# Optimization experiments

Measured on AMD Instinct MI355X. Metric: run time of the kernel, lower is better.

Reference implementation:

```python
import jax, jax.numpy as jnp
import numpy as np

BS, NQ, L = 64, 900, 1024
LANG_DIM, HID = 768, 256
N_EXP, TOP_K = 8, 2
MOE_W = 0.5
LOG_SCALE0 = 0.0
PRIOR_PROB = 0.01
BIAS0 = -np.log((1.0 - PRIOR_PROB) / PRIOR_PROB)  # -log((1-p)/p)


def setup_inputs() -> dict:
    key = jax.random.key(0)
    ks = jax.random.split(key, 8)
    s_in = 1.0 / np.sqrt(LANG_DIM)
    return {
        "x": jax.random.normal(ks[0], (BS, NQ, HID), jnp.float32),
        "embedding": jax.random.normal(ks[1], (BS, L, LANG_DIM), jnp.float32),
        "proj_w": jax.random.uniform(ks[2], (LANG_DIM, HID), jnp.float32, -s_in, s_in),
        "proj_b": jnp.zeros((HID,), jnp.float32),
        "gate_w": jax.random.uniform(ks[3], (LANG_DIM, N_EXP), jnp.float32, -s_in, s_in),
        "gate_b": jnp.zeros((N_EXP,), jnp.float32),
        "expert_w": jax.random.uniform(ks[4], (N_EXP, LANG_DIM, HID), jnp.float32, -s_in, s_in),
        "expert_b": jnp.zeros((N_EXP, HID), jnp.float32),
        "bias_lang": jnp.zeros((LANG_DIM,), jnp.float32),
        "bias0": jnp.array([BIAS0], jnp.float32),
        "log_scale": jnp.array([LOG_SCALE0], jnp.float32),
    }


def _moe(emb, gate_w, gate_b, expert_w, expert_b):
    # emb: (bs, L, lang_dim)
    gate_logits = emb @ gate_w + gate_b              # (bs, L, E)
    gate_weights = jax.nn.softmax(gate_logits, axis=-1)
    topv, topi = jax.lax.top_k(gate_weights, TOP_K)  # (bs, L, k)
    # dense combine weights: scatter top-k probs back to (bs, L, E)
    combine = jnp.sum(jax.nn.one_hot(topi, N_EXP, dtype=emb.dtype) * topv[..., None], axis=-2)
    out = jnp.zeros(emb.shape[:-1] + (HID,), emb.dtype)
    for e in range(N_EXP):  # small fixed expert count; dense per-expert GEMM
        out = out + combine[..., e:e + 1] * (emb @ expert_w[e] + expert_b[e])
    return out


def reference(x, embedding, proj_w, proj_b, gate_w, gate_b,
              expert_w, expert_b, bias_lang, bias0, log_scale):
    emb = embedding / jnp.linalg.norm(embedding, axis=-1, keepdims=True)
    tokens = emb @ proj_w + proj_b                        # (bs, L, HID)
    moe_out = _moe(emb, gate_w, gate_b, expert_w, expert_b)
    tokens = (1.0 - MOE_W) * tokens + MOE_W * moe_out
    token_bias = emb @ bias_lang + bias0[0]               # (bs, L)
    logit = jnp.einsum('bqh,blh->bql', x, tokens) / jnp.exp(log_scale[0])
    logit = logit + token_bias[:, None, :]
    logit = jnp.clip(logit, -50000.0, 50000.0)
    return logit
```

## Files before the change

kernel.cpp:

```cpp
#include <hip/hip_runtime.h>
#include <hip/hip_bf16.h>


typedef __attribute__((ext_vector_type(8))) short bf16x8;
typedef __attribute__((ext_vector_type(4))) float f32x4;

#define NROW 65536
#define CAP  65536
#define CSTRIDE 16
#define SWZ(r) ((((r) & 3) ^ (((r) >> 2) & 3)))

__device__ __forceinline__ unsigned short f2bf(float f) {
    unsigned u = __builtin_bit_cast(unsigned, f);
    u += 0x7fffu + ((u >> 16) & 1u);
    return (unsigned short)(u >> 16);
}
__device__ __forceinline__ float bf2f(unsigned short h) {
    unsigned u = ((unsigned)h) << 16;
    return __builtin_bit_cast(float, u);
}
__device__ __forceinline__ void gload16(const void* g, void* l) {
    __builtin_amdgcn_global_load_lds(
        (const __attribute__((address_space(1))) void*)g,
        (__attribute__((address_space(3))) void*)l, 16, 0, 0);
}
__device__ __forceinline__ unsigned cvt_pk_bf16(float a, float b) {
    unsigned r;
    asm("v_cvt_pk_bf16_f32 %0, %1, %2" : "=v"(r) : "v"(a), "v"(b));
    return r;
}

__global__ __launch_bounds__(256) void kx_cast(
    const float* __restrict__ x, unsigned short* __restrict__ x_bf)
{
    int i = blockIdx.x * 256 + threadIdx.x;
    float4 v = ((const float4*)x)[i];
    unsigned long long o = (unsigned long long)cvt_pk_bf16(v.x, v.y) |
                           ((unsigned long long)cvt_pk_bf16(v.z, v.w) << 32);
    __builtin_nontemporal_store(o, (unsigned long long*)x_bf + i);
}

__global__ __launch_bounds__(256) void k0_wT(
    const float* __restrict__ proj_w, const float* __restrict__ expert_w,
    unsigned short* __restrict__ wcatT)
{
    int j = blockIdx.z;
    int d0 = blockIdx.x * 64, h0 = blockIdx.y * 64;
    const float* W = (j < 8) ? expert_w + (size_t)j * 768 * 256 : proj_w;
    __shared__ unsigned short s[64][65];
    int t = threadIdx.x;
    #pragma unroll
    for (int i = 0; i < 16; i++) {
        int d = i * 4 + (t >> 6), h = t & 63;
        s[d][h] = f2bf(W[(size_t)(d0 + d) * 256 + h0 + h]);
    }
    __syncthreads();
    #pragma unroll
    for (int i = 0; i < 16; i++) {
        int h = i * 4 + (t >> 6), d = t & 63;
        wcatT[(size_t)(j * 256 + h0 + h) * 768 + d0 + d] = s[d][h];
    }
}

__global__ __launch_bounds__(256) void kz_misc(
    const float* __restrict__ proj_b, const float* __restrict__ expert_b,
    float* __restrict__ bcat, unsigned* __restrict__ cnt)
{
    int i = blockIdx.x * 256 + threadIdx.x;
    if (i < 2304) {
        int jj = i >> 8, h = i & 255;
        bcat[i] = (jj < 8) ? expert_b[jj * 256 + h] : proj_b[h];
    }
    if (i < 8 * CSTRIDE) cnt[i] = 0;
}

__global__ __launch_bounds__(256, 4) void k1_fused(
    const float* __restrict__ emb_in, const float* __restrict__ gate_w,
    const float* __restrict__ gate_b, const float* __restrict__ bias_lang,
    const float* __restrict__ bias0, unsigned short* __restrict__ emb_bf,
    unsigned* __restrict__ top2, float2* __restrict__ c2,
    float* __restrict__ tbias)
{
    __shared__ float gwT[9 * 768];
    for (int i = threadIdx.x; i < 768 * 8; i += 256) {
        int d = i >> 3, e = i & 7;
        gwT[e * 768 + d] = gate_w[i];
    }
    for (int i = threadIdx.x; i < 768; i += 256)
        gwT[8 * 768 + i] = bias_lang[i];
    __syncthreads();

    int w = threadIdx.x >> 6, lane = threadIdx.x & 63;
    #pragma unroll 1
    for (int it = 0; it < 8; ++it) {
        int r = blockIdx.x * 32 + w * 8 + it;
        const float4* rv = (const float4*)(emb_in + (size_t)r * 768);
        float4 v0 = rv[lane], v1 = rv[lane + 64], v2 = rv[lane + 128];
        float ss = v0.x*v0.x + v0.y*v0.y + v0.z*v0.z + v0.w*v0.w
                 + v1.x*v1.x + v1.y*v1.y + v1.z*v1.z + v1.w*v1.w
                 + v2.x*v2.x + v2.y*v2.y + v2.z*v2.z + v2.w*v2.w;
        #pragma unroll
        for (int m = 1; m < 64; m <<= 1) ss += __shfl_xor(ss, m, 64);
        float rn = rsqrtf(ss);

        unsigned long long q0 = (unsigned long long)cvt_pk_bf16(v0.x*rn, v0.y*rn) |
                                ((unsigned long long)cvt_pk_bf16(v0.z*rn, v0.w*rn) << 32);
        unsigned long long q1 = (unsigned long long)cvt_pk_bf16(v1.x*rn, v1.y*rn) |
                                ((unsigned long long)cvt_pk_bf16(v1.z*rn, v1.w*rn) << 32);
        unsigned long long q2 = (unsigned long long)cvt_pk_bf16(v2.x*rn, v2.y*rn) |
                                ((unsigned long long)cvt_pk_bf16(v2.z*rn, v2.w*rn) << 32);
        unsigned long long* ob = (unsigned long long*)(emb_bf + (size_t)r * 768);
        __builtin_nontemporal_store(q0, ob + lane);
        __builtin_nontemporal_store(q1, ob + lane + 64);
        __builtin_nontemporal_store(q2, ob + lane + 128);

        float acc[9];
        #pragma unroll
        for (int i = 0; i < 9; i++) acc[i] = 0.f;
        const float4 vv[3] = { v0, v1, v2 };
        #pragma unroll
        for (int k = 0; k < 3; k++) {
            float4 v = vv[k];
            #pragma unroll
            for (int e = 0; e < 9; e++) {
                float4 g = *(const float4*)&gwT[e * 768 + k * 256 + lane * 4];
                acc[e] += v.x*g.x + v.y*g.y + v.z*g.z + v.w*g.w;
            }
        }
        #pragma unroll
        for (int m = 1; m < 64; m <<= 1) {
            #pragma unroll
            for (int i = 0; i < 9; i++) acc[i] += __shfl_xor(acc[i], m, 64);
        }
        if (lane == 0) {
            float g[8];
            #pragma unroll
            for (int e = 0; e < 8; e++) g[e] = acc[e] * rn + gate_b[e];
            float mx = g[0];
            #pragma unroll
            for (int e = 1; e < 8; e++) mx = fmaxf(mx, g[e]);
            float p[8], s = 0.f;
            #pragma unroll
            for (int e = 0; e < 8; e++) { p[e] = __expf(g[e] - mx); s += p[e]; }
            float inv = 0.5f / s;
            int i1 = 0;
            #pragma unroll
            for (int e = 1; e < 8; e++) if (g[e] > g[i1]) i1 = e;
            int i2 = (i1 == 0) ? 1 : 0;
            #pragma unroll
            for (int e = 0; e < 8; e++) if (e != i1 && g[e] > g[i2]) i2 = e;
            top2[r] = (unsigned)i1 | ((unsigned)i2 << 8);
            c2[r]   = make_float2(p[i1] * inv, p[i2] * inv);
            tbias[r] = acc[8] * rn + bias0[0];
        }
    }
}

__global__ __launch_bounds__(256) void kb_bucket(
    const unsigned* __restrict__ top2, const float2* __restrict__ c2,
    unsigned* __restrict__ cnt, unsigned* __restrict__ bidx,
    float* __restrict__ bscale)
{
    __shared__ unsigned lcnt[8];
    __shared__ unsigned gbase[8];
    int tid = threadIdx.x, lane = tid & 63;
    if (tid < 8) lcnt[tid] = 0;
    __syncthreads();
    int r = blockIdx.x * 256 + tid;
    unsigned t = top2[r];
    float2 c = c2[r];
    int ii[2] = { (int)(t & 255), (int)((t >> 8) & 255) };
    float cc[2] = { c.x, c.y };
    unsigned lpos[2];
    #pragma unroll
    for (int slot = 0; slot < 2; slot++) {
        int myE = ii[slot];
        #pragma unroll 1
        for (int e = 0; e < 8; e++) {
            unsigned long long mask = __ballot(myE == e);
            if (myE == e) {
                int leader = __ffsll((unsigned long long)mask) - 1;
                unsigned base = 0;
                if (lane == leader)
                    base = atomicAdd(&lcnt[e], (unsigned)__popcll(mask));
                base = __shfl(base, leader, 64);
                lpos[slot] = base + (unsigned)__popcll(mask & ((1ull << lane) - 1ull));
            }
        }
    }
    __syncthreads();
    if (tid < 8) gbase[tid] = atomicAdd(&cnt[tid * CSTRIDE], lcnt[tid]);
    __syncthreads();
    #pragma unroll
    for (int slot = 0; slot < 2; slot++) {
        int e = ii[slot];
        unsigned p = gbase[e] + lpos[slot];
        bidx[(size_t)e * CAP + p]   = (unsigned)r | ((unsigned)slot << 16);
        bscale[(size_t)e * CAP + p] = cc[slot];
    }
}

__global__ __launch_bounds__(512, 2) void k2_expert(
    const unsigned short* __restrict__ emb_bf, const unsigned short* __restrict__ wcatT,
    const float* __restrict__ bcat, const unsigned* __restrict__ cnt,
    const unsigned* __restrict__ bidx, const float* __restrict__ bscale,
    unsigned short* __restrict__ partial)
{
    int e = blockIdx.y;
    int tile = blockIdx.x;
    int cnt_e = (int)cnt[e * CSTRIDE];
    if (tile * 128 >= cnt_e) return;
    int tid = threadIdx.x, lane = tid & 63, w = tid >> 6;
    int wm = w >> 2, wn = w & 3;
    __shared__ __align__(16) unsigned short As[2][128 * 32];
    __shared__ __align__(16) unsigned short Bs[2][256 * 32];
    __shared__ unsigned sRow[128];
    __shared__ float sScale[128];
    if (tid < 128) {
        int gi = tile * 128 + tid;
        unsigned rs; float sc;
        if (gi < cnt_e) { rs = bidx[(size_t)e * CAP + gi];
                          sc = bscale[(size_t)e * CAP + gi]; }
        else            { rs = 0; sc = 0.f; }
        sRow[tid] = rs; sScale[tid] = sc;
    }
    __syncthreads();
    int r16 = lane & 15, r4 = lane >> 4;
    int srowA = tid >> 2, ssegA = (tid & 3) ^ SWZ(srowA);
    const unsigned short* aSrc =
        emb_bf + (size_t)(sRow[srowA] & 0xFFFFu) * 768 + ssegA * 8;
    const unsigned short* bBase = wcatT + (size_t)e * 256 * 768;

    auto stageA = [&](int kt, int buf) {
        gload16(aSrc + kt * 32, &As[buf][w * 512]);
    };
    auto stageB = [&](int kt, int buf) {
        #pragma unroll
        for (int i = 0; i < 2; i++) {
            int u = i * 512 + tid;
            int brow = u >> 2, seg = (u & 3) ^ SWZ(brow);
            gload16(&bBase[(size_t)brow * 768 + kt * 32 + seg * 8],
                    &Bs[buf][i * 4096 + w * 512]);
        }
    };

    f32x4 acc[4][4];
    #pragma unroll
    for (int mi = 0; mi < 4; mi++)
        #pragma unroll
        for (int ni = 0; ni < 4; ni++) acc[mi][ni] = f32x4{0.f, 0.f, 0.f, 0.f};

    stageA(0, 0); stageB(0, 0);
    __syncthreads();
    int buf = 0;
    #pragma unroll 1
    for (int kt = 0; kt < 24; ++kt) {
        if (kt < 23) { stageA(kt + 1, buf ^ 1); stageB(kt + 1, buf ^ 1); }
        bf16x8 a[4], b[4];
        #pragma unroll
        for (int mi = 0; mi < 4; mi++) {
            int arow = wm * 64 + mi * 16 + r16;
            a[mi] = *(const bf16x8*)&As[buf][arow * 32 + (r4 ^ SWZ(arow)) * 8];
        }
        #pragma unroll
        for (int ni = 0; ni < 4; ni++) {
            int brow = wn * 64 + ni * 16 + r16;
            b[ni] = *(const bf16x8*)&Bs[buf][brow * 32 + (r4 ^ SWZ(brow)) * 8];
        }
        #pragma unroll
        for (int mi = 0; mi < 4; mi++)
            #pragma unroll
            for (int ni = 0; ni < 4; ni++)
                acc[mi][ni] = __builtin_amdgcn_mfma_f32_16x16x32_bf16(
                    a[mi], b[ni], acc[mi][ni], 0, 0, 0);
        __syncthreads();
        buf ^= 1;
    }

    float bj[4];
    #pragma unroll
    for (int ni = 0; ni < 4; ni++) bj[ni] = bcat[e * 256 + wn * 64 + ni * 16 + r16];
    #pragma unroll
    for (int mi = 0; mi < 4; mi++) {
        #pragma unroll
        for (int e4 = 0; e4 < 4; e4++) {
            int rl = wm * 64 + mi * 16 + r4 * 4 + e4;
            if (tile * 128 + rl < cnt_e) {
                unsigned rs = sRow[rl];
                float sc = sScale[rl];
                unsigned rowg = rs & 0xFFFFu, slot = rs >> 16;
                #pragma unroll
                for (int ni = 0; ni < 4; ni++) {
                    int col = wn * 64 + ni * 16 + r16;
                    __builtin_nontemporal_store(
                        f2bf(sc * (acc[mi][ni][e4] + bj[ni])),
                        &partial[((size_t)slot * NROW + rowg) * 256 + col]);
                }
            }
        }
    }
}

__global__ __launch_bounds__(512, 2) void k2_proj(
    const unsigned short* __restrict__ emb_bf, const unsigned short* __restrict__ wcatT,
    const float* __restrict__ bcat, const unsigned short* __restrict__ partial,
    unsigned short* __restrict__ tokens)
{
    int tile = blockIdx.x;
    int tid = threadIdx.x, lane = tid & 63, w = tid >> 6;
    int wm = w >> 2, wn = w & 3;
    int rowBase = tile * 128;
    __shared__ __align__(16) unsigned short As[2][128 * 32];
    __shared__ __align__(16) unsigned short Bs[2][256 * 32];
    int r16 = lane & 15, r4 = lane >> 4;
    int srowA = tid >> 2, ssegA = (tid & 3) ^ SWZ(srowA);
    const unsigned short* aSrc =
        emb_bf + (size_t)(rowBase + srowA) * 768 + ssegA * 8;
    const unsigned short* bBase = wcatT + (size_t)8 * 256 * 768;

    auto stageA = [&](int kt, int buf) {
        gload16(aSrc + kt * 32, &As[buf][w * 512]);
    };
    auto stageB = [&](int kt, int buf) {
        #pragma unroll
        for (int i = 0; i < 2; i++) {
            int u = i * 512 + tid;
            int brow = u >> 2, seg = (u & 3) ^ SWZ(brow);
            gload16(&bBase[(size_t)brow * 768 + kt * 32 + seg * 8],
                    &Bs[buf][i * 4096 + w * 512]);
        }
    };

    f32x4 acc[4][4];
    #pragma unroll
    for (int mi = 0; mi < 4; mi++)
        #pragma unroll
        for (int ni = 0; ni < 4; ni++) acc[mi][ni] = f32x4{0.f, 0.f, 0.f, 0.f};

    stageA(0, 0); stageB(0, 0);
    __syncthreads();
    int buf = 0;
    #pragma unroll 1
    for (int kt = 0; kt < 24; ++kt) {
        if (kt < 23) { stageA(kt + 1, buf ^ 1); stageB(kt + 1, buf ^ 1); }
        bf16x8 a[4], b[4];
        #pragma unroll
        for (int mi = 0; mi < 4; mi++) {
            int arow = wm * 64 + mi * 16 + r16;
            a[mi] = *(const bf16x8*)&As[buf][arow * 32 + (r4 ^ SWZ(arow)) * 8];
        }
        #pragma unroll
        for (int ni = 0; ni < 4; ni++) {
            int brow = wn * 64 + ni * 16 + r16;
            b[ni] = *(const bf16x8*)&Bs[buf][brow * 32 + (r4 ^ SWZ(brow)) * 8];
        }
        #pragma unroll
        for (int mi = 0; mi < 4; mi++)
            #pragma unroll
            for (int ni = 0; ni < 4; ni++)
                acc[mi][ni] = __builtin_amdgcn_mfma_f32_16x16x32_bf16(
                    a[mi], b[ni], acc[mi][ni], 0, 0, 0);
        __syncthreads();
        buf ^= 1;
    }

    const size_t S = (size_t)NROW * 256;
    float bj[4];
    #pragma unroll
    for (int ni = 0; ni < 4; ni++) bj[ni] = bcat[8 * 256 + wn * 64 + ni * 16 + r16];
    #pragma unroll
    for (int mi = 0; mi < 4; mi++) {
        #pragma unroll
        for (int e4 = 0; e4 < 4; e4++) {
            int rl = wm * 64 + mi * 16 + r4 * 4 + e4;
            size_t rowg = rowBase + rl;
            #pragma unroll
            for (int ni = 0; ni < 4; ni++) {
                int col = wn * 64 + ni * 16 + r16;
                float p0 = bf2f(partial[rowg * 256 + col]);
                float p1 = bf2f(partial[S + rowg * 256 + col]);
                float v = 0.5f * (acc[mi][ni][e4] + bj[ni]) + p0 + p1;
                __builtin_nontemporal_store(f2bf(v), &tokens[rowg * 256 + col]);
            }
        }
    }
}

__global__ __launch_bounds__(256, 4) void k3_logit(
    const unsigned short* __restrict__ x_bf, const unsigned short* __restrict__ tokens,
    const float* __restrict__ tbias, const float* __restrict__ log_scale,
    float* __restrict__ out)
{
    int tid = threadIdx.x, lane = tid & 63, w = tid >> 6;
    int wm = w >> 1, wn = w & 1;
    int tn = blockIdx.x, tm = blockIdx.y, b = blockIdx.z;
    __shared__ __align__(16) unsigned short As[2][128 * 32];
    __shared__ __align__(16) unsigned short Bs[2][128 * 32];
    const unsigned short* A = x_bf + (size_t)b * 900 * 256;
    const unsigned short* B = tokens + (size_t)b * 1024 * 256;
    f32x4 acc[4][4];
    #pragma unroll
    for (int mi = 0; mi < 4; mi++)
        #pragma unroll
        for (int ni = 0; ni < 4; ni++) acc[mi][ni] = f32x4{0.f, 0.f, 0.f, 0.f};
    int r16 = lane & 15, r4 = lane >> 4;

    auto stage = [&](int kt, int buf) {
        #pragma unroll
        for (int i = 0; i < 2; i++) {
            int u = i * 256 + tid;
            int row = u >> 2, seg = (u & 3) ^ SWZ(row);
            int ar = tm * 128 + row;
            if (ar > 899) ar = 899;
            gload16(&A[(size_t)ar * 256 + kt * 32 + seg * 8],
                    &As[buf][i * 2048 + w * 512]);
            int nr = tn * 128 + row;
            gload16(&B[(size_t)nr * 256 + kt * 32 + seg * 8],
                    &Bs[buf][i * 2048 + w * 512]);
        }
    };

    stage(0, 0);
    __syncthreads();
    int buf = 0;
    #pragma unroll 1
    for (int kt = 0; kt < 8; ++kt) {
        if (kt < 7) stage(kt + 1, buf ^ 1);
        bf16x8 a[4], bb[4];
        #pragma unroll
        for (int mi = 0; mi < 4; mi++) {
            int row = wm * 64 + mi * 16 + r16;
            a[mi] = *(const bf16x8*)&As[buf][row * 32 + (r4 ^ SWZ(row)) * 8];
        }
        #pragma unroll
        for (int ni = 0; ni < 4; ni++) {
            int row = wn * 64 + ni * 16 + r16;
            bb[ni] = *(const bf16x8*)&Bs[buf][row * 32 + (r4 ^ SWZ(row)) * 8];
        }
        #pragma unroll
        for (int mi = 0; mi < 4; mi++)
            #pragma unroll
            for (int ni = 0; ni < 4; ni++)
                acc[mi][ni] = __builtin_amdgcn_mfma_f32_16x16x32_bf16(
                    a[mi], bb[ni], acc[mi][ni], 0, 0, 0);
        __syncthreads();
        buf ^= 1;
    }
    float inv = __expf(-log_scale[0]);
    #pragma unroll
    for (int ni = 0; ni < 4; ni++) {
        int l = tn * 128 + wn * 64 + ni * 16 + r16;
        float tbv = tbias[b * 1024 + l];
        #pragma unroll
        for (int mi = 0; mi < 4; mi++) {
            #pragma unroll
            for (int e = 0; e < 4; e++) {
                int q = tm * 128 + wm * 64 + mi * 16 + r4 * 4 + e;
                if (q < 900) {
                    float vv = acc[mi][ni][e] * inv + tbv;
                    vv = fminf(fmaxf(vv, -50000.f), 50000.f);
                    __builtin_nontemporal_store(
                        vv, &out[((size_t)b * 900 + q) * 1024 + l]);
                }
            }
        }
    }
}

extern "C" void kernel_launch(void* const* d_in, const int* in_sizes, int n_in,
                              void* d_out, int out_size, void* d_ws, size_t ws_size,
                              hipStream_t stream)
{
    const float* x         = (const float*)d_in[0];
    const float* embedding = (const float*)d_in[1];
    const float* proj_w    = (const float*)d_in[2];
    const float* proj_b    = (const float*)d_in[3];
    const float* gate_w    = (const float*)d_in[4];
    const float* gate_b    = (const float*)d_in[5];
    const float* expert_w  = (const float*)d_in[6];
    const float* expert_b  = (const float*)d_in[7];
    const float* bias_lang = (const float*)d_in[8];
    const float* bias0     = (const float*)d_in[9];
    const float* log_scale = (const float*)d_in[10];
    float* out = (float*)d_out;

    size_t off = 0;
    char* base = (char*)d_ws;
    auto alloc = [&](size_t bytes) -> void* {
        void* p = base + off;
        off += (bytes + 255) & ~(size_t)255;
        return p;
    };
    unsigned short* emb_bf  = (unsigned short*)alloc((size_t)NROW * 768 * 2);
    unsigned short* x_bf    = (unsigned short*)alloc((size_t)14745600 * 2);
    unsigned short* wcatT   = (unsigned short*)alloc((size_t)2304 * 768 * 2);
    float* bcat             = (float*)alloc(2304 * 4);
    float* tbias            = (float*)alloc((size_t)NROW * 4);
    unsigned short* tokens  = (unsigned short*)alloc((size_t)NROW * 256 * 2);
    unsigned* cnt           = (unsigned*)alloc(8 * CSTRIDE * 4);
    unsigned* top2          = (unsigned*)alloc((size_t)NROW * 4);
    float2* c2              = (float2*)alloc((size_t)NROW * 8);
    unsigned* bidx          = (unsigned*)alloc((size_t)8 * CAP * 4);
    float* bscale           = (float*)alloc((size_t)8 * CAP * 4);
    unsigned short* partial = (unsigned short*)alloc((size_t)2 * NROW * 256 * 2);

    kx_cast<<<14400, 256, 0, stream>>>(x, x_bf);
    dim3 gt(12, 4, 9);
    k0_wT<<<gt, 256, 0, stream>>>(proj_w, expert_w, wcatT);
    kz_misc<<<9, 256, 0, stream>>>(proj_b, expert_b, bcat, cnt);
    k1_fused<<<2048, 256, 0, stream>>>(embedding, gate_w, gate_b, bias_lang, bias0,
                                       emb_bf, top2, c2, tbias);
    kb_bucket<<<NROW / 256, 256, 0, stream>>>(top2, c2, cnt, bidx, bscale);
    dim3 g2(512, 8);
    k2_expert<<<g2, 512, 0, stream>>>(emb_bf, wcatT, bcat, cnt, bidx, bscale, partial);
    k2_proj<<<512, 512, 0, stream>>>(emb_bf, wcatT, bcat, partial, tokens);
    dim3 g3(8, 8, 64);
    k3_logit<<<g3, 256, 0, stream>>>(x_bf, tokens, tbias, log_scale, out);
}
```

Measured before the change: 393.8 us.

## Enlarge GEMM block tiles to 256 rows in expert, proj and logit kernels

Doubles the M tile of the expert and projection GEMMs from 128 to 256 rows. Each warp now holds 8x4 accumulators, and A fragments are loaded inside the mi loop. The logit kernel moves from 128x128 tiles with 256 threads to 256x256 tiles with 512 threads. The aim is to raise operand reuse per LDS load and cut global traffic per output. The cost is higher register and LDS use, fewer blocks (hurting occupancy and tail balance on sparse expert buckets), and more wasted work on the padded 900-row edge of the logit GEMM.

```diff
diff --git a/kernel.cpp b/kernel.cpp
--- a/kernel.cpp
+++ b/kernel.cpp
@@ -209,15 +209,18 @@
     int e = blockIdx.y;
     int tile = blockIdx.x;
     int cnt_e = (int)cnt[e * CSTRIDE];
-    if (tile * 128 >= cnt_e) return;
+    if (tile * 256 >= cnt_e) return;
     int tid = threadIdx.x, lane = tid & 63, w = tid >> 6;
     int wm = w >> 2, wn = w & 3;
-    __shared__ __align__(16) unsigned short As[2][128 * 32];
+    __shared__ __align__(16) unsigned short As[2][256 * 32];
     __shared__ __align__(16) unsigned short Bs[2][256 * 32];
-    __shared__ unsigned sRow[128];
-    __shared__ float sScale[128];
-    if (tid < 128) {
-        int gi = tile * 128 + tid;
+    __shared__ unsigned sRow[256];
+    __shared__ float sScale[256];
+    #pragma unroll
+    for (int i = 0; i < 1; i++) {
+    }
+    if (tid < 256) {
+        int gi = tile * 256 + tid;
         unsigned rs; float sc;
         if (gi < cnt_e) { rs = bidx[(size_t)e * CAP + gi];
                           sc = bscale[(size_t)e * CAP + gi]; }
@@ -226,13 +229,17 @@
     }
     __syncthreads();
     int r16 = lane & 15, r4 = lane >> 4;
-    int srowA = tid >> 2, ssegA = (tid & 3) ^ SWZ(srowA);
-    const unsigned short* aSrc =
-        emb_bf + (size_t)(sRow[srowA] & 0xFFFFu) * 768 + ssegA * 8;
+    int row0 = tid >> 2, row1 = 128 + (tid >> 2);
+    int seg0 = (tid & 3) ^ SWZ(row0), seg1 = (tid & 3) ^ SWZ(row1);
+    const unsigned short* aSrc0 =
+        emb_bf + (size_t)(sRow[row0] & 0xFFFFu) * 768 + seg0 * 8;
+    const unsigned short* aSrc1 =
+        emb_bf + (size_t)(sRow[row1] & 0xFFFFu) * 768 + seg1 * 8;
     const unsigned short* bBase = wcatT + (size_t)e * 256 * 768;
 
     auto stageA = [&](int kt, int buf) {
-        gload16(aSrc + kt * 32, &As[buf][w * 512]);
+        gload16(aSrc0 + kt * 32, &As[buf][w * 512]);
+        gload16(aSrc1 + kt * 32, &As[buf][4096 + w * 512]);
     };
     auto stageB = [&](int kt, int buf) {
         #pragma unroll
@@ -244,9 +251,9 @@
         }
     };
 
-    f32x4 acc[4][4];
-    #pragma unroll
-    for (int mi = 0; mi < 4; mi++)
+    f32x4 acc[8][4];
+    #pragma unroll
+    for (int mi = 0; mi < 8; mi++)
         #pragma unroll
         for (int ni = 0; ni < 4; ni++) acc[mi][ni] = f32x4{0.f, 0.f, 0.f, 0.f};
 
@@ -256,23 +263,21 @@
     #pragma unroll 1
     for (int kt = 0; kt < 24; ++kt) {
         if (kt < 23) { stageA(kt + 1, buf ^ 1); stageB(kt + 1, buf ^ 1); }
-        bf16x8 a[4], b[4];
-        #pragma unroll
-        for (int mi = 0; mi < 4; mi++) {
-            int arow = wm * 64 + mi * 16 + r16;
-            a[mi] = *(const bf16x8*)&As[buf][arow * 32 + (r4 ^ SWZ(arow)) * 8];
-        }
+        bf16x8 b[4];
         #pragma unroll
         for (int ni = 0; ni < 4; ni++) {
             int brow = wn * 64 + ni * 16 + r16;
             b[ni] = *(const bf16x8*)&Bs[buf][brow * 32 + (r4 ^ SWZ(brow)) * 8];
         }
         #pragma unroll
-        for (int mi = 0; mi < 4; mi++)
+        for (int mi = 0; mi < 8; mi++) {
+            int arow = wm * 128 + mi * 16 + r16;
+            bf16x8 a = *(const bf16x8*)&As[buf][arow * 32 + (r4 ^ SWZ(arow)) * 8];
             #pragma unroll
             for (int ni = 0; ni < 4; ni++)
                 acc[mi][ni] = __builtin_amdgcn_mfma_f32_16x16x32_bf16(
-                    a[mi], b[ni], acc[mi][ni], 0, 0, 0);
+                    a, b[ni], acc[mi][ni], 0, 0, 0);
+        }
         __syncthreads();
         buf ^= 1;
     }
@@ -281,11 +286,11 @@
     #pragma unroll
     for (int ni = 0; ni < 4; ni++) bj[ni] = bcat[e * 256 + wn * 64 + ni * 16 + r16];
     #pragma unroll
-    for (int mi = 0; mi < 4; mi++) {
+    for (int mi = 0; mi < 8; mi++) {
         #pragma unroll
         for (int e4 = 0; e4 < 4; e4++) {
-            int rl = wm * 64 + mi * 16 + r4 * 4 + e4;
-            if (tile * 128 + rl < cnt_e) {
+            int rl = wm * 128 + mi * 16 + r4 * 4 + e4;
+            if (tile * 256 + rl < cnt_e) {
                 unsigned rs = sRow[rl];
                 float sc = sScale[rl];
                 unsigned rowg = rs & 0xFFFFu, slot = rs >> 16;
@@ -309,17 +314,21 @@
     int tile = blockIdx.x;
     int tid = threadIdx.x, lane = tid & 63, w = tid >> 6;
     int wm = w >> 2, wn = w & 3;
-    int rowBase = tile * 128;
-    __shared__ __align__(16) unsigned short As[2][128 * 32];
+    int rowBase = tile * 256;
+    __shared__ __align__(16) unsigned short As[2][256 * 32];
     __shared__ __align__(16) unsigned short Bs[2][256 * 32];
     int r16 = lane & 15, r4 = lane >> 4;
-    int srowA = tid >> 2, ssegA = (tid & 3) ^ SWZ(srowA);
-    const unsigned short* aSrc =
-        emb_bf + (size_t)(rowBase + srowA) * 768 + ssegA * 8;
+    int row0 = tid >> 2, row1 = 128 + (tid >> 2);
+    int seg0 = (tid & 3) ^ SWZ(row0), seg1 = (tid & 3) ^ SWZ(row1);
+    const unsigned short* aSrc0 =
+        emb_bf + (size_t)(rowBase + row0) * 768 + seg0 * 8;
+    const unsigned short* aSrc1 =
+        emb_bf + (size_t)(rowBase + row1) * 768 + seg1 * 8;
     const unsigned short* bBase = wcatT + (size_t)8 * 256 * 768;
 
     auto stageA = [&](int kt, int buf) {
-        gload16(aSrc + kt * 32, &As[buf][w * 512]);
+        gload16(aSrc0 + kt * 32, &As[buf][w * 512]);
+        gload16(aSrc1 + kt * 32, &As[buf][4096 + w * 512]);
     };
     auto stageB = [&](int kt, int buf) {
         #pragma unroll
@@ -331,9 +340,9 @@
         }
     };
 
-    f32x4 acc[4][4];
-    #pragma unroll
-    for (int mi = 0; mi < 4; mi++)
+    f32x4 acc[8][4];
+    #pragma unroll
+    for (int mi = 0; mi < 8; mi++)
         #pragma unroll
         for (int ni = 0; ni < 4; ni++) acc[mi][ni] = f32x4{0.f, 0.f, 0.f, 0.f};
 
@@ -343,23 +352,21 @@
     #pragma unroll 1
     for (int kt = 0; kt < 24; ++kt) {
         if (kt < 23) { stageA(kt + 1, buf ^ 1); stageB(kt + 1, buf ^ 1); }
-        bf16x8 a[4], b[4];
-        #pragma unroll
-        for (int mi = 0; mi < 4; mi++) {
-            int arow = wm * 64 + mi * 16 + r16;
-            a[mi] = *(const bf16x8*)&As[buf][arow * 32 + (r4 ^ SWZ(arow)) * 8];
-        }
+        bf16x8 b[4];
         #pragma unroll
         for (int ni = 0; ni < 4; ni++) {
             int brow = wn * 64 + ni * 16 + r16;
             b[ni] = *(const bf16x8*)&Bs[buf][brow * 32 + (r4 ^ SWZ(brow)) * 8];
         }
         #pragma unroll
-        for (int mi = 0; mi < 4; mi++)
+        for (int mi = 0; mi < 8; mi++) {
+            int arow = wm * 128 + mi * 16 + r16;
+            bf16x8 a = *(const bf16x8*)&As[buf][arow * 32 + (r4 ^ SWZ(arow)) * 8];
             #pragma unroll
             for (int ni = 0; ni < 4; ni++)
                 acc[mi][ni] = __builtin_amdgcn_mfma_f32_16x16x32_bf16(
-                    a[mi], b[ni], acc[mi][ni], 0, 0, 0);
+                    a, b[ni], acc[mi][ni], 0, 0, 0);
+        }
         __syncthreads();
         buf ^= 1;
     }
@@ -369,10 +376,10 @@
     #pragma unroll
     for (int ni = 0; ni < 4; ni++) bj[ni] = bcat[8 * 256 + wn * 64 + ni * 16 + r16];
     #pragma unroll
-    for (int mi = 0; mi < 4; mi++) {
+    for (int mi = 0; mi < 8; mi++) {
         #pragma unroll
         for (int e4 = 0; e4 < 4; e4++) {
-            int rl = wm * 64 + mi * 16 + r4 * 4 + e4;
+            int rl = wm * 128 + mi * 16 + r4 * 4 + e4;
             size_t rowg = rowBase + rl;
             #pragma unroll
             for (int ni = 0; ni < 4; ni++) {
@@ -386,21 +393,21 @@
     }
 }
 
-__global__ __launch_bounds__(256, 4) void k3_logit(
+__global__ __launch_bounds__(512, 2) void k3_logit(
     const unsigned short* __restrict__ x_bf, const unsigned short* __restrict__ tokens,
     const float* __restrict__ tbias, const float* __restrict__ log_scale,
     float* __restrict__ out)
 {
     int tid = threadIdx.x, lane = tid & 63, w = tid >> 6;
-    int wm = w >> 1, wn = w & 1;
+    int wm = w >> 2, wn = w & 3;
     int tn = blockIdx.x, tm = blockIdx.y, b = blockIdx.z;
-    __shared__ __align__(16) unsigned short As[2][128 * 32];
-    __shared__ __align__(16) unsigned short Bs[2][128 * 32];
+    __shared__ __align__(16) unsigned short As[2][256 * 32];
+    __shared__ __align__(16) unsigned short Bs[2][256 * 32];
     const unsigned short* A = x_bf + (size_t)b * 900 * 256;
     const unsigned short* B = tokens + (size_t)b * 1024 * 256;
-    f32x4 acc[4][4];
-    #pragma unroll
-    for (int mi = 0; mi < 4; mi++)
+    f32x4 acc[8][4];
+    #pragma unroll
+    for (int mi = 0; mi < 8; mi++)
         #pragma unroll
         for (int ni = 0; ni < 4; ni++) acc[mi][ni] = f32x4{0.f, 0.f, 0.f, 0.f};
     int r16 = lane & 15, r4 = lane >> 4;
@@ -408,15 +415,15 @@
     auto stage = [&](int kt, int buf) {
         #pragma unroll
         for (int i = 0; i < 2; i++) {
-            int u = i * 256 + tid;
+            int u = i * 512 + tid;
             int row = u >> 2, seg = (u & 3) ^ SWZ(row);
-            int ar = tm * 128 + row;
+            int ar = tm * 256 + row;
             if (ar > 899) ar = 899;
             gload16(&A[(size_t)ar * 256 + kt * 32 + seg * 8],
-                    &As[buf][i * 2048 + w * 512]);
-            int nr = tn * 128 + row;
+                    &As[buf][i * 4096 + w * 512]);
+            int nr = tn * 256 + row;
             gload16(&B[(size_t)nr * 256 + kt * 32 + seg * 8],
-                    &Bs[buf][i * 2048 + w * 512]);
+                    &Bs[buf][i * 4096 + w * 512]);
         }
     };
 
@@ -426,36 +433,34 @@
     #pragma unroll 1
     for (int kt = 0; kt < 8; ++kt) {
         if (kt < 7) stage(kt + 1, buf ^ 1);
-        bf16x8 a[4], bb[4];
-        #pragma unroll
-        for (int mi = 0; mi < 4; mi++) {
-            int row = wm * 64 + mi * 16 + r16;
-            a[mi] = *(const bf16x8*)&As[buf][row * 32 + (r4 ^ SWZ(row)) * 8];
-        }
+        bf16x8 bb[4];
         #pragma unroll
         for (int ni = 0; ni < 4; ni++) {
             int row = wn * 64 + ni * 16 + r16;
             bb[ni] = *(const bf16x8*)&Bs[buf][row * 32 + (r4 ^ SWZ(row)) * 8];
         }
         #pragma unroll
-        for (int mi = 0; mi < 4; mi++)
+        for (int mi = 0; mi < 8; mi++) {
+            int row = wm * 128 + mi * 16 + r16;
+            bf16x8 a = *(const bf16x8*)&As[buf][row * 32 + (r4 ^ SWZ(row)) * 8];
             #pragma unroll
             for (int ni = 0; ni < 4; ni++)
                 acc[mi][ni] = __builtin_amdgcn_mfma_f32_16x16x32_bf16(
-                    a[mi], bb[ni], acc[mi][ni], 0, 0, 0);
+                    a, bb[ni], acc[mi][ni], 0, 0, 0);
+        }
         __syncthreads();
         buf ^= 1;
     }
     float inv = __expf(-log_scale[0]);
     #pragma unroll
     for (int ni = 0; ni < 4; ni++) {
-        int l = tn * 128 + wn * 64 + ni * 16 + r16;
+        int l = tn * 256 + wn * 64 + ni * 16 + r16;
         float tbv = tbias[b * 1024 + l];
         #pragma unroll
-        for (int mi = 0; mi < 4; mi++) {
+        for (int mi = 0; mi < 8; mi++) {
             #pragma unroll
             for (int e = 0; e < 4; e++) {
-                int q = tm * 128 + wm * 64 + mi * 16 + r4 * 4 + e;
+                int q = tm * 256 + wm * 128 + mi * 16 + r4 * 4 + e;
                 if (q < 900) {
                     float vv = acc[mi][ni][e] * inv + tbv;
                     vv = fminf(fmaxf(vv, -50000.f), 50000.f);
@@ -511,9 +516,9 @@
     k1_fused<<<2048, 256, 0, stream>>>(embedding, gate_w, gate_b, bias_lang, bias0,
                                        emb_bf, top2, c2, tbias);
     kb_bucket<<<NROW / 256, 256, 0, stream>>>(top2, c2, cnt, bidx, bscale);
-    dim3 g2(512, 8);
+    dim3 g2(256, 8);
     k2_expert<<<g2, 512, 0, stream>>>(emb_bf, wcatT, bcat, cnt, bidx, bscale, partial);
-    k2_proj<<<512, 512, 0, stream>>>(emb_bf, wcatT, bcat, partial, tokens);
-    dim3 g3(8, 8, 64);
-    k3_logit<<<g3, 256, 0, stream>>>(x_bf, tokens, tbias, log_scale, out);
-}
+    k2_proj<<<256, 512, 0, stream>>>(emb_bf, wcatT, bcat, partial, tokens);
+    dim3 g3(4, 4, 64);
+    k3_logit<<<g3, 512, 0, stream>>>(x_bf, tokens, tbias, log_scale, out);
+}
```

Result: slower. 412.2 us (+4.7%).

## Restructure logit GEMM to keep A fragments in registers and stream B directly

Applied to the files above, without the earlier changes.

Rewrites k3_logit so each block handles 64 query rows and all 1024 tokens. Each wave keeps the full K=256 A fragments in registers and streams token rows straight from global memory in 32-column chunks, with no LDS staging and no block syncs. This removes the LDS round-trip and barrier overhead and reads x only once per query tile. In exchange it adds register pressure, lowering occupancy to 2 blocks per SIMD, and B loads become uncoalesced global reads that depend on cache.

```diff
diff --git a/kernel.cpp b/kernel.cpp
--- a/kernel.cpp
+++ b/kernel.cpp
@@ -386,81 +386,67 @@
     }
 }
 
-__global__ __launch_bounds__(256, 4) void k3_logit(
+__global__ __launch_bounds__(256, 2) void k3_logit(
     const unsigned short* __restrict__ x_bf, const unsigned short* __restrict__ tokens,
     const float* __restrict__ tbias, const float* __restrict__ log_scale,
     float* __restrict__ out)
 {
-    int tid = threadIdx.x, lane = tid & 63, w = tid >> 6;
-    int wm = w >> 1, wn = w & 1;
-    int tn = blockIdx.x, tm = blockIdx.y, b = blockIdx.z;
-    __shared__ __align__(16) unsigned short As[2][128 * 32];
-    __shared__ __align__(16) unsigned short Bs[2][128 * 32];
+    int lane = threadIdx.x & 63, w = threadIdx.x >> 6;
+    int tm = blockIdx.x, b = blockIdx.y;
+    int r16 = lane & 15, r4 = lane >> 4;
+    int qBase = tm * 64;
     const unsigned short* A = x_bf + (size_t)b * 900 * 256;
-    const unsigned short* B = tokens + (size_t)b * 1024 * 256;
-    f32x4 acc[4][4];
-    #pragma unroll
-    for (int mi = 0; mi < 4; mi++)
-        #pragma unroll
-        for (int ni = 0; ni < 4; ni++) acc[mi][ni] = f32x4{0.f, 0.f, 0.f, 0.f};
-    int r16 = lane & 15, r4 = lane >> 4;
-
-    auto stage = [&](int kt, int buf) {
-        #pragma unroll
-        for (int i = 0; i < 2; i++) {
-            int u = i * 256 + tid;
-            int row = u >> 2, seg = (u & 3) ^ SWZ(row);
-            int ar = tm * 128 + row;
-            if (ar > 899) ar = 899;
-            gload16(&A[(size_t)ar * 256 + kt * 32 + seg * 8],
-                    &As[buf][i * 2048 + w * 512]);
-            int nr = tn * 128 + row;
-            gload16(&B[(size_t)nr * 256 + kt * 32 + seg * 8],
-                    &Bs[buf][i * 2048 + w * 512]);
-        }
-    };
-
-    stage(0, 0);
-    __syncthreads();
-    int buf = 0;
+    const unsigned short* B = tokens + ((size_t)b * 1024 + (size_t)w * 256) * 256;
+
+    bf16x8 af[4][8];
+    #pragma unroll
+    for (int mi = 0; mi < 4; mi++) {
+        int q = qBase + mi * 16 + r16;
+        if (q > 899) q = 899;
+        const unsigned short* ap = A + (size_t)q * 256 + r4 * 8;
+        #pragma unroll
+        for (int kt = 0; kt < 8; kt++)
+            af[mi][kt] = *(const bf16x8*)(ap + kt * 32);
+    }
+    float inv = __expf(-log_scale[0]);
+
     #pragma unroll 1
-    for (int kt = 0; kt < 8; ++kt) {
-        if (kt < 7) stage(kt + 1, buf ^ 1);
-        bf16x8 a[4], bb[4];
-        #pragma unroll
-        for (int mi = 0; mi < 4; mi++) {
-            int row = wm * 64 + mi * 16 + r16;
-            a[mi] = *(const bf16x8*)&As[buf][row * 32 + (r4 ^ SWZ(row)) * 8];
-        }
-        #pragma unroll
-        for (int ni = 0; ni < 4; ni++) {
-            int row = wn * 64 + ni * 16 + r16;
-            bb[ni] = *(const bf16x8*)&Bs[buf][row * 32 + (r4 ^ SWZ(row)) * 8];
-        }
+    for (int c = 0; c < 8; c++) {
+        f32x4 acc[4][2];
         #pragma unroll
         for (int mi = 0; mi < 4; mi++)
             #pragma unroll
-            for (int ni = 0; ni < 4; ni++)
-                acc[mi][ni] = __builtin_amdgcn_mfma_f32_16x16x32_bf16(
-                    a[mi], bb[ni], acc[mi][ni], 0, 0, 0);
-        __syncthreads();
-        buf ^= 1;
-    }
-    float inv = __expf(-log_scale[0]);
-    #pragma unroll
-    for (int ni = 0; ni < 4; ni++) {
-        int l = tn * 128 + wn * 64 + ni * 16 + r16;
-        float tbv = tbias[b * 1024 + l];
-        #pragma unroll
-        for (int mi = 0; mi < 4; mi++) {
-            #pragma unroll
-            for (int e = 0; e < 4; e++) {
-                int q = tm * 128 + wm * 64 + mi * 16 + r4 * 4 + e;
-                if (q < 900) {
-                    float vv = acc[mi][ni][e] * inv + tbv;
-                    vv = fminf(fmaxf(vv, -50000.f), 50000.f);
-                    __builtin_nontemporal_store(
-                        vv, &out[((size_t)b * 900 + q) * 1024 + l]);
+            for (int ni = 0; ni < 2; ni++) acc[mi][ni] = f32x4{0.f, 0.f, 0.f, 0.f};
+        #pragma unroll
+        for (int kt = 0; kt < 8; kt++) {
+            bf16x8 bfr[2];
+            #pragma unroll
+            for (int ni = 0; ni < 2; ni++) {
+                int lloc = c * 32 + ni * 16 + r16;
+                bfr[ni] = *(const bf16x8*)(B + (size_t)lloc * 256 + kt * 32 + r4 * 8);
+            }
+            #pragma unroll
+            for (int mi = 0; mi < 4; mi++)
+                #pragma unroll
+                for (int ni = 0; ni < 2; ni++)
+                    acc[mi][ni] = __builtin_amdgcn_mfma_f32_16x16x32_bf16(
+                        af[mi][kt], bfr[ni], acc[mi][ni], 0, 0, 0);
+        }
+        #pragma unroll
+        for (int ni = 0; ni < 2; ni++) {
+            int l = w * 256 + c * 32 + ni * 16 + r16;
+            float tbv = tbias[b * 1024 + l];
+            #pragma unroll
+            for (int mi = 0; mi < 4; mi++) {
+                #pragma unroll
+                for (int e = 0; e < 4; e++) {
+                    int q = qBase + mi * 16 + r4 * 4 + e;
+                    if (q < 900) {
+                        float vv = acc[mi][ni][e] * inv + tbv;
+                        vv = fminf(fmaxf(vv, -50000.f), 50000.f);
+                        __builtin_nontemporal_store(
+                            vv, &out[((size_t)b * 900 + q) * 1024 + l]);
+                    }
                 }
             }
         }
@@ -514,6 +500,6 @@
     dim3 g2(512, 8);
     k2_expert<<<g2, 512, 0, stream>>>(emb_bf, wcatT, bcat, cnt, bidx, bscale, partial);
     k2_proj<<<512, 512, 0, stream>>>(emb_bf, wcatT, bcat, partial, tokens);
-    dim3 g3(8, 8, 64);
+    dim3 g3(15, 64);
     k3_logit<<<g3, 256, 0, stream>>>(x_bf, tokens, tbias, log_scale, out);
 }
```

Result: slower. 449.0 us (+14.0%).
